# Optimization experiments

Measured on AMD Instinct MI355X. Metric: run time of the kernel, lower is better.

Reference implementation:

```python
import jax, jax.numpy as jnp
import numpy as np

B, N, K, DEG = 128, 4096, 25, 16
BN_EPS = 1e-5


def setup_inputs() -> dict:
    key = jax.random.key(0)
    ks = jax.random.split(key, 16)

    def sp_lap(k, V):
        # fixed-degree random sparse scaled Laplacian (COO); values scaled so the
        # K=25 Chebyshev recursion x2 = 2*L@x1 - x0 stays numerically bounded
        rows = jnp.repeat(jnp.arange(V, dtype=jnp.int32), DEG)
        cols = jax.random.randint(k, (V * DEG,), 0, V, dtype=jnp.int32)
        vals = jax.random.normal(jax.random.fold_in(k, 1), (V * DEG,), jnp.float32) * 0.05
        return rows, cols, vals

    l0_rows, l0_cols, l0_vals = sp_lap(ks[0], N)
    l2_rows, l2_cols, l2_vals = sp_lap(ks[1], N // 4)
    l4_rows, l4_cols, l4_vals = sp_lap(ks[2], N // 16)

    x = jax.random.normal(ks[3], (B, N, 1), jnp.float32)
    w1 = jax.random.normal(ks[4], (1 * K, 32), jnp.float32) * 0.1
    b1 = jnp.zeros((32,), jnp.float32)
    w2 = jax.random.normal(ks[5], (32 * K, 64), jnp.float32) * 0.05
    b2 = jnp.zeros((64,), jnp.float32)
    w3 = jax.random.normal(ks[6], (64 * K, 64), jnp.float32) * 0.05
    b3 = jnp.zeros((64,), jnp.float32)
    fc1_w = jax.random.normal(ks[7], (N // 16 * 64, 512), jnp.float32) * 0.01
    fc1_b = jnp.zeros((512,), jnp.float32)
    bn_gamma = jnp.ones((512,), jnp.float32)
    bn_beta = jnp.zeros((512,), jnp.float32)
    fc2_w = jax.random.normal(ks[8], (512, 10), jnp.float32) * 0.05
    fc2_b = jnp.zeros((10,), jnp.float32)

    return dict(x=x,
                l0_rows=l0_rows, l0_cols=l0_cols, l0_vals=l0_vals,
                l2_rows=l2_rows, l2_cols=l2_cols, l2_vals=l2_vals,
                l4_rows=l4_rows, l4_cols=l4_cols, l4_vals=l4_vals,
                w1=w1, b1=b1, w2=w2, b2=b2, w3=w3, b3=b3,
                fc1_w=fc1_w, fc1_b=fc1_b, bn_gamma=bn_gamma, bn_beta=bn_beta,
                fc2_w=fc2_w, fc2_b=fc2_b)


def spmm(rows, cols, vals, xm, V):
    # sparse (V,V) @ dense (V,M) via gather + segment-sum
    return jax.ops.segment_sum(vals[:, None] * xm[cols], rows, num_segments=V)


def cheb(rows, cols, vals, x, W, b):
    # GCNCheb: Chebyshev polynomial basis T_k(L) x, k=0..K-1, then linear projection
    Bb, V, Fin = x.shape
    Kk = W.shape[0] // Fin
    x0 = jnp.transpose(x, (1, 2, 0)).reshape(V, Fin * Bb)  # (V, Fin*B)
    xs = [x0]
    x1 = spmm(rows, cols, vals, x0, V)
    xs.append(x1)
    for _ in range(2, Kk):
        x2 = 2.0 * spmm(rows, cols, vals, x1, V) - x0
        xs.append(x2)
        x0, x1 = x1, x2
    Xc = jnp.stack(xs, 0).reshape(Kk, V, Fin, Bb)          # (K, V, Fin, B)
    Xc = jnp.transpose(Xc, (3, 1, 2, 0)).reshape(Bb * V, Fin * Kk)
    return (Xc @ W + b).reshape(Bb, V, -1)


def pool4(x):
    # max-pool over consecutive groups of 4 nodes (gcn_pool_4)
    Bb, V, F = x.shape
    return x.reshape(Bb, V // 4, 4, F).max(axis=2)


def reference(x,
              l0_rows, l0_cols, l0_vals,
              l2_rows, l2_cols, l2_vals,
              l4_rows, l4_cols, l4_vals,
              w1, b1, w2, b2, w3, b3,
              fc1_w, fc1_b, bn_gamma, bn_beta, fc2_w, fc2_b):
    h = jax.nn.relu(cheb(l0_rows, l0_cols, l0_vals, x, w1, b1))
    h = pool4(h)                                             # (B, N/4, 32)
    h = jax.nn.relu(cheb(l2_rows, l2_cols, l2_vals, h, w2, b2))
    h = pool4(h)                                             # (B, N/16, 64)
    h = jax.nn.relu(cheb(l4_rows, l4_cols, l4_vals, h, w3, b3))
    h = h.reshape(h.shape[0], -1)                            # (B, N/16 * 64)
    h = h @ fc1_w + fc1_b                                    # (B, 512)
    mean = h.mean(axis=0)
    var = h.var(axis=0)  # biased, matching torch BatchNorm training normalization
    h = (h - mean) / jnp.sqrt(var + BN_EPS) * bn_gamma + bn_beta
    h = jax.nn.relu(h)
    logits = h @ fc2_w + fc2_b                               # (B, 10)
    return jax.nn.log_softmax(logits, axis=1)
```

## Files before the change

kernel.cpp:

```cpp
#include <hip/hip_runtime.h>

#define B_ 128
#define K_ 25
#define DEG_ 16

#define R4(X) X(0) X(1) X(2) X(3)

typedef __attribute__((ext_vector_type(4))) float f32x4;
typedef __attribute__((ext_vector_type(8))) short bf16x8;

__device__ __forceinline__ float4 f4ma(float t, float4 w, float4 a) {
    a.x = fmaf(t, w.x, a.x); a.y = fmaf(t, w.y, a.y);
    a.z = fmaf(t, w.z, a.z); a.w = fmaf(t, w.w, a.w);
    return a;
}
__device__ __forceinline__ float4 f4max(float4 a, float4 b) {
    return make_float4(fmaxf(a.x, b.x), fmaxf(a.y, b.y), fmaxf(a.z, b.z), fmaxf(a.w, b.w));
}
__device__ __forceinline__ unsigned f2bfu(float f) {
    unsigned u = __float_as_uint(f);
    return (u + 0x7FFFu + ((u >> 16) & 1u)) >> 16;
}
__device__ __forceinline__ unsigned packbf(float e, float o) { return f2bfu(e) | (f2bfu(o) << 16); }

__device__ __forceinline__ bf16x8 u2b(uint4 u) {
    union { uint4 u4; bf16x8 b8; } c; c.u4 = u; return c.b8;
}
__device__ __forceinline__ f32x4 mfma_bf(uint4 a, uint4 b, f32x4 c) {
    return __builtin_amdgcn_mfma_f32_16x16x32_bf16(u2b(a), u2b(b), c, 0, 0, 0);
}

__global__ __launch_bounds__(256) void k_transpose_x(const float* __restrict__ x, float* __restrict__ x0) {
    int i = blockIdx.x * 256 + threadIdx.x;
    int v = i >> 7, b = i & 127;
    x0[i] = x[(b << 12) + v];
}

__global__ __launch_bounds__(256) void k_packw(const float* __restrict__ w2, const float* __restrict__ w3,
        unsigned short* __restrict__ wb2, unsigned short* __restrict__ wb3) {
    int i = blockIdx.x * 256 + threadIdx.x;
    if (i < 51200) {
        int k = i >> 11, rem = i & 2047, fo = rem >> 5, fi = rem & 31;
        wb2[i] = (unsigned short)f2bfu(w2[(size_t)(fi * K_ + k) * 64 + fo]);
    }
    if (i < 102400) {
        int k = i >> 12, rem = i & 4095, fo = rem >> 6, fi = rem & 63;
        wb3[i] = (unsigned short)f2bfu(w3[(size_t)(fi * K_ + k) * 64 + fo]);
    }
}

__global__ __launch_bounds__(256) void k_spmm1(const int* __restrict__ cols, const float* __restrict__ vals,
        const float2* __restrict__ cur, const float2* __restrict__ prev,
        float2* __restrict__ next, int two) {
    int t = blockIdx.x * 256 + threadIdx.x;
    int v = __builtin_amdgcn_readfirstlane(t >> 6);
    int lane = threadIdx.x & 63;
    int base = v * DEG_;
    float2 s = make_float2(0.f, 0.f);
#pragma unroll
    for (int d = 0; d < DEG_; ++d) {
        float wv = vals[base + d];
        float2 xx = cur[((size_t)cols[base + d] << 6) + lane];
        s.x = fmaf(wv, xx.x, s.x); s.y = fmaf(wv, xx.y, s.y);
    }
    size_t idx = ((size_t)v << 6) + lane;
    if (two) {
        float2 p = prev[idx];
        s.x = 2.f * s.x - p.x; s.y = 2.f * s.y - p.y;
    }
    next[idx] = s;
}

template<int LOGC4>
__global__ __launch_bounds__(256) void k_spmm4(const int* __restrict__ cols, const float* __restrict__ vals,
                        const float4* __restrict__ cur, const float4* __restrict__ prev,
                        float4* __restrict__ next, unsigned* __restrict__ mir, int two) {
    constexpr int LOGW4 = LOGC4 - 3;
    int xcd = blockIdx.x & 7, q = blockIdx.x >> 3;
    int tid = q * 256 + threadIdx.x;
    int v = __builtin_amdgcn_readfirstlane(tid >> LOGW4);
    int c4 = (xcd << LOGW4) + (tid & ((1 << LOGW4) - 1));
    int base = v * DEG_;
    float4 s = make_float4(0.f, 0.f, 0.f, 0.f);
#pragma unroll
    for (int d = 0; d < DEG_; ++d) {
        float w = vals[base + d];
        float4 xx = cur[((size_t)cols[base + d] << LOGC4) + c4];
        s = f4ma(w, xx, s);
    }
    size_t idx = ((size_t)v << LOGC4) + c4;
    if (two) {
        float4 p = prev[idx];
        s.x = 2.f * s.x - p.x; s.y = 2.f * s.y - p.y;
        s.z = 2.f * s.z - p.z; s.w = 2.f * s.w - p.w;
    }
    next[idx] = s;
    float tx = __shfl_down(s.x, 32), ty = __shfl_down(s.y, 32),
          tz = __shfl_down(s.z, 32), tw = __shfl_down(s.w, 32);
    if ((threadIdx.x & 63) < 32) {
        int c = c4 << 2;
        int fi2 = c >> 8, b0 = c & 127;
        uint4 m = make_uint4(packbf(s.x, tx), packbf(s.y, ty), packbf(s.z, tz), packbf(s.w, tw));
        *(uint4*)(mir + ((size_t)v << (LOGC4 + 1)) + ((size_t)fi2 << 7) + b0) = m;
    }
}

__global__ __launch_bounds__(256) void k_proj1_pool(const float* __restrict__ basis,
        const float* __restrict__ W1, const float* __restrict__ b1, float* __restrict__ pool1,
        unsigned* __restrict__ mir) {
    int half = blockIdx.y;
    int i = blockIdx.x * 256 + threadIdx.x;
    int g = i >> 7, b = i & 127;
    const float* wbase = W1 + half * 16;
#define P1_DM(j) float4 M##j = make_float4(-1e30f, -1e30f, -1e30f, -1e30f);
    R4(P1_DM)
#undef P1_DM
    for (int r = 0; r < 4; ++r) {
        const float* bp = basis + (((size_t)(4 * g + r) << 7) + b);
#define P1_DC(j) float4 C##j = make_float4(0.f, 0.f, 0.f, 0.f);
        R4(P1_DC)
#undef P1_DC
#pragma unroll 5
        for (int k = 0; k < K_; ++k) {
            float tv = bp[(size_t)k * 524288];
            const float4* w = (const float4*)(wbase + k * 32);
#define P1_FM(j) C##j = f4ma(tv, w[j], C##j);
            R4(P1_FM)
#undef P1_FM
        }
#define P1_MX(j) M##j = f4max(M##j, C##j);
        R4(P1_MX)
#undef P1_MX
    }
    float* op = pool1 + ((size_t)g << 12) + ((size_t)half << 11) + b;
    unsigned* mp = mir + ((size_t)g << 11) + ((size_t)half << 10) + b;
    const float* bb = b1 + half * 16;
#define P1_ST(j) { \
    float e0 = fmaxf(M##j.x + bb[4*j+0], 0.f); \
    float o0 = fmaxf(M##j.y + bb[4*j+1], 0.f); \
    float e1 = fmaxf(M##j.z + bb[4*j+2], 0.f); \
    float o1 = fmaxf(M##j.w + bb[4*j+3], 0.f); \
    op[(4*j+0)*128] = e0; op[(4*j+1)*128] = o0; \
    op[(4*j+2)*128] = e1; op[(4*j+3)*128] = o1; \
    mp[(2*j+0)*128] = packbf(e0, o0); \
    mp[(2*j+1)*128] = packbf(e1, o1); }
    R4(P1_ST)
#undef P1_ST
}

__global__ __launch_bounds__(256) void k_proj_l2m(const unsigned* __restrict__ mir, size_t slotH,
        const uint4* __restrict__ wb, float* __restrict__ acc, int k0, int init,
        const float* __restrict__ bias) {
    int wid = blockIdx.x * 4 + (threadIdx.x >> 6);
    int lane = threadIdx.x & 63;
    int lm = lane & 15, lg = lane >> 4;
    int v = wid >> 3, b0 = (wid & 7) << 4;
    float* ap = acc + ((size_t)v << 13) + b0 + (lg << 2);
    f32x4 C0, C1, C2, C3;
    if (init) {
        float q0 = bias[lm], q1 = bias[16 + lm], q2 = bias[32 + lm], q3 = bias[48 + lm];
        C0 = f32x4{q0, q0, q0, q0}; C1 = f32x4{q1, q1, q1, q1};
        C2 = f32x4{q2, q2, q2, q2}; C3 = f32x4{q3, q3, q3, q3};
    } else {
        C0 = *(const f32x4*)(ap + (size_t)lm * 128);
        C1 = *(const f32x4*)(ap + (size_t)(16 + lm) * 128);
        C2 = *(const f32x4*)(ap + (size_t)(32 + lm) * 128);
        C3 = *(const f32x4*)(ap + (size_t)(48 + lm) * 128);
    }
    const unsigned* mp0 = mir + ((size_t)v << 11) + (lg << 9) + b0 + lm;
#pragma unroll
    for (int kk = 0; kk < 5; ++kk) {
        const unsigned* mp = mp0 + (size_t)kk * slotH;
        uint4 a = make_uint4(mp[0], mp[128], mp[256], mp[384]);
        int kb = (k0 + kk) << 6;
        uint4 w0 = wb[(kb + lm) * 4 + lg];
        uint4 w1 = wb[(kb + 16 + lm) * 4 + lg];
        uint4 w2 = wb[(kb + 32 + lm) * 4 + lg];
        uint4 w3 = wb[(kb + 48 + lm) * 4 + lg];
        C0 = mfma_bf(a, w0, C0);
        C1 = mfma_bf(a, w1, C1);
        C2 = mfma_bf(a, w2, C2);
        C3 = mfma_bf(a, w3, C3);
    }
    *(f32x4*)(ap + (size_t)lm * 128) = C0;
    *(f32x4*)(ap + (size_t)(16 + lm) * 128) = C1;
    *(f32x4*)(ap + (size_t)(32 + lm) * 128) = C2;
    *(f32x4*)(ap + (size_t)(48 + lm) * 128) = C3;
}

__global__ __launch_bounds__(256) void k_proj_l3m(const unsigned* __restrict__ mir, size_t slotH,
        const uint4* __restrict__ wb, float* __restrict__ acc, int k0, int init,
        const float* __restrict__ bias, int finalrelu) {
    int wid = blockIdx.x * 4 + (threadIdx.x >> 6);
    int lane = threadIdx.x & 63;
    int lm = lane & 15, lg = lane >> 4;
    int v = wid >> 3, b0 = (wid & 7) << 4;
    float* ap = acc + ((size_t)v << 13) + b0 + (lg << 2);
    f32x4 C0, C1, C2, C3;
    if (init) {
        float q0 = bias[lm], q1 = bias[16 + lm], q2 = bias[32 + lm], q3 = bias[48 + lm];
        C0 = f32x4{q0, q0, q0, q0}; C1 = f32x4{q1, q1, q1, q1};
        C2 = f32x4{q2, q2, q2, q2}; C3 = f32x4{q3, q3, q3, q3};
    } else {
        C0 = *(const f32x4*)(ap + (size_t)lm * 128);
        C1 = *(const f32x4*)(ap + (size_t)(16 + lm) * 128);
        C2 = *(const f32x4*)(ap + (size_t)(32 + lm) * 128);
        C3 = *(const f32x4*)(ap + (size_t)(48 + lm) * 128);
    }
    const unsigned* mp0 = mir + ((size_t)v << 12) + b0 + lm;
#pragma unroll
    for (int kk = 0; kk < 5; ++kk) {
        const unsigned* mp = mp0 + (size_t)kk * slotH;
        int kb = (k0 + kk) << 6;
#pragma unroll
        for (int ks = 0; ks < 2; ++ks) {
            const unsigned* mk = mp + (size_t)((ks << 4) + (lg << 2)) * 128;
            uint4 a = make_uint4(mk[0], mk[128], mk[256], mk[384]);
            int wof = (ks << 2) + lg;
            uint4 w0 = wb[(kb + lm) * 8 + wof];
            uint4 w1 = wb[(kb + 16 + lm) * 8 + wof];
            uint4 w2 = wb[(kb + 32 + lm) * 8 + wof];
            uint4 w3 = wb[(kb + 48 + lm) * 8 + wof];
            C0 = mfma_bf(a, w0, C0);
            C1 = mfma_bf(a, w1, C1);
            C2 = mfma_bf(a, w2, C2);
            C3 = mfma_bf(a, w3, C3);
        }
    }
    if (finalrelu) {
#pragma unroll
        for (int r = 0; r < 4; ++r) {
            C0[r] = fmaxf(C0[r], 0.f); C1[r] = fmaxf(C1[r], 0.f);
            C2[r] = fmaxf(C2[r], 0.f); C3[r] = fmaxf(C3[r], 0.f);
        }
    }
    *(f32x4*)(ap + (size_t)lm * 128) = C0;
    *(f32x4*)(ap + (size_t)(16 + lm) * 128) = C1;
    *(f32x4*)(ap + (size_t)(32 + lm) * 128) = C2;
    *(f32x4*)(ap + (size_t)(48 + lm) * 128) = C3;
}

__global__ __launch_bounds__(256) void k_relu_pool_m(const float* __restrict__ acc,
        float* __restrict__ pool, unsigned* __restrict__ mir) {
    int i = blockIdx.x * 256 + threadIdx.x;
    int g = i >> 12, fi2 = (i >> 7) & 31, b = i & 127;
    const float* ap = acc + (((size_t)g << 2) << 13) + (fi2 << 8) + b;
    float me = 0.f, mo = 0.f;
#pragma unroll
    for (int r = 0; r < 4; ++r) {
        me = fmaxf(me, ap[0]); mo = fmaxf(mo, ap[128]);
        ap += 8192;
    }
    size_t po = ((size_t)g << 13) + (fi2 << 8) + b;
    pool[po] = me; pool[po + 128] = mo;
    mir[i] = packbf(me, mo);
}

__global__ __launch_bounds__(256) void k_fc1_part(const float* __restrict__ t3, const float* __restrict__ w,
                           float* __restrict__ part) {
    int blk = blockIdx.x;
    int bg = blk >> 7;
    int rs = (blk >> 1) & 63;
    int j = ((blk & 1) << 8) + threadIdx.x;
    int b0 = bg << 3;
    float a0=0.f,a1=0.f,a2=0.f,a3=0.f,a4=0.f,a5=0.f,a6=0.f,a7=0.f;
    int r0 = rs << 8;
#pragma unroll 4
    for (int row = r0; row < r0 + 256; ++row) {
        float wv = w[((size_t)row << 9) + j];
        const float4* tp = (const float4*)(t3 + ((size_t)row << 7) + b0);
        float4 t0 = tp[0], t1 = tp[1];
        a0 = fmaf(t0.x, wv, a0);
        a1 = fmaf(t0.y, wv, a1);
        a2 = fmaf(t0.z, wv, a2);
        a3 = fmaf(t0.w, wv, a3);
        a4 = fmaf(t1.x, wv, a4);
        a5 = fmaf(t1.y, wv, a5);
        a6 = fmaf(t1.z, wv, a6);
        a7 = fmaf(t1.w, wv, a7);
    }
    float* pp = part + (((size_t)(rs << 7) + b0) << 9) + j;
    pp[0*512]=a0; pp[1*512]=a1; pp[2*512]=a2; pp[3*512]=a3;
    pp[4*512]=a4; pp[5*512]=a5; pp[6*512]=a6; pp[7*512]=a7;
}

__global__ __launch_bounds__(256) void k_fc1_red(const float* __restrict__ part, const float* __restrict__ bias,
                          float* __restrict__ h) {
    int i = blockIdx.x * 256 + threadIdx.x;
    float a = bias[i & 511];
#pragma unroll 8
    for (int rs = 0; rs < 64; ++rs) a += part[((size_t)rs << 16) + i];
    h[i] = a;
}

__global__ void k_bnstats(const float* __restrict__ h, float* __restrict__ mv) {
    __shared__ float s1[128], s2[128];
    int j = blockIdx.x, t = threadIdx.x;
    float v = h[(size_t)t * 512 + j];
    s1[t] = v; s2[t] = v * v;
    __syncthreads();
    for (int o = 64; o > 0; o >>= 1) {
        if (t < o) { s1[t] += s1[t + o]; s2[t] += s2[t + o]; }
        __syncthreads();
    }
    if (t == 0) {
        float m = s1[0] * (1.f / 128.f);
        float var = s2[0] * (1.f / 128.f) - m * m;
        mv[j] = m;
        mv[512 + j] = rsqrtf(var + 1e-5f);
    }
}

__global__ void k_head(const float* __restrict__ h, const float* __restrict__ mv,
                       const float* __restrict__ gamma, const float* __restrict__ beta,
                       const float* __restrict__ w2, const float* __restrict__ b2,
                       float* __restrict__ out) {
    __shared__ float hr[512];
    __shared__ float lg[16];
    int b = blockIdx.x, t = threadIdx.x;
    for (int j = t; j < 512; j += 64) {
        float x = (h[(size_t)b * 512 + j] - mv[j]) * mv[512 + j] * gamma[j] + beta[j];
        hr[j] = fmaxf(x, 0.f);
    }
    __syncthreads();
    if (t < 10) {
        float a = b2[t];
        for (int j = 0; j < 512; ++j) a += hr[j] * w2[j * 10 + t];
        lg[t] = a;
    }
    __syncthreads();
    if (t == 0) {
        float mx = -1e30f;
        for (int q = 0; q < 10; ++q) mx = fmaxf(mx, lg[q]);
        float sum = 0.f;
        for (int q = 0; q < 10; ++q) sum += expf(lg[q] - mx);
        float ls = logf(sum) + mx;
        for (int q = 0; q < 10; ++q) out[b * 10 + q] = lg[q] - ls;
    }
}

extern "C" void kernel_launch(void* const* d_in, const int* in_sizes, int n_in,
                              void* d_out, int out_size, void* d_ws, size_t ws_size,
                              hipStream_t stream) {
    (void)in_sizes; (void)n_in; (void)out_size; (void)ws_size;
    const float* x      = (const float*)d_in[0];
    const int*   l0cols = (const int*)d_in[2];
    const float* l0vals = (const float*)d_in[3];
    const int*   l2cols = (const int*)d_in[5];
    const float* l2vals = (const float*)d_in[6];
    const int*   l4cols = (const int*)d_in[8];
    const float* l4vals = (const float*)d_in[9];
    const float* w1   = (const float*)d_in[10];
    const float* b1   = (const float*)d_in[11];
    const float* w2   = (const float*)d_in[12];
    const float* b2   = (const float*)d_in[13];
    const float* w3   = (const float*)d_in[14];
    const float* b3   = (const float*)d_in[15];
    const float* fc1w = (const float*)d_in[16];
    const float* fc1b = (const float*)d_in[17];
    const float* gam  = (const float*)d_in[18];
    const float* bet  = (const float*)d_in[19];
    const float* fc2w = (const float*)d_in[20];
    const float* fc2b = (const float*)d_in[21];
    float* out = (float*)d_out;

    const size_t S1 = 4096 * 128;
    const size_t S2 = 1024 * 4096;
    const size_t S3 = 256 * 8192;
    const int CKP = 5;

    float* ws = (float*)d_ws;
    float* basis1 = ws;
    float* ring2f = ws + 25 * S1;
    unsigned* mir2 = (unsigned*)(ring2f + 3 * S2);
    float* tailp  = (float*)(mir2 + (size_t)CKP * (S2 / 2));
    float* h      = tailp;
    float* mv     = h + 65536;
    unsigned short* wb2 = (unsigned short*)(mv + 1024);
    unsigned short* wb3 = wb2 + 51200;
    float* acc2   = basis1;
    float* ring3f = ring2f;
    float* acc3   = ring2f + 3 * S3;
    unsigned* mir3 = mir2;
    float* part   = basis1;

    k_packw<<<400, 256, 0, stream>>>(w2, w3, wb2, wb3);

    k_transpose_x<<<2048, 256, 0, stream>>>(x, basis1);
    for (int k = 1; k < 25; ++k) {
        const float* cur  = basis1 + (size_t)(k - 1) * S1;
        const float* prev = (k >= 2) ? basis1 + (size_t)(k - 2) * S1 : cur;
        float* next = basis1 + (size_t)k * S1;
        k_spmm1<<<1024, 256, 0, stream>>>(l0cols, l0vals, (const float2*)cur,
                                          (const float2*)prev, (float2*)next, k >= 2 ? 1 : 0);
    }
    k_proj1_pool<<<dim3(512, 2), 256, 0, stream>>>(basis1, w1, b1, ring2f, mir2);

    {
        int cs = 0;
        for (int k = 0; k < 25; ++k) {
            if (k >= 1) {
                const float* cur  = ring2f + (size_t)((k - 1) % 3) * S2;
                const float* prev = ring2f + (size_t)((k >= 2 ? k - 2 : 0) % 3) * S2;
                float* next = ring2f + (size_t)(k % 3) * S2;
                unsigned* mirp = mir2 + (size_t)(k % CKP) * (S2 / 2);
                k_spmm4<10><<<4096, 256, 0, stream>>>(l2cols, l2vals, (const float4*)cur,
                                                      (const float4*)prev, (float4*)next,
                                                      mirp, k >= 2 ? 1 : 0);
            }
            if (k - cs + 1 == CKP) {
                k_proj_l2m<<<2048, 256, 0, stream>>>(mir2, S2 / 2, (const uint4*)wb2, acc2, cs,
                                                     cs == 0 ? 1 : 0, b2);
                cs = k + 1;
            }
        }
    }
    k_relu_pool_m<<<4096, 256, 0, stream>>>(acc2, ring3f , mir3 );

    {
        int cs = 0;
        for (int k = 0; k < 25; ++k) {
            if (k >= 1) {
                const float* cur  = ring3f + (size_t)((k - 1) % 3) * S3;
                const float* prev = ring3f + (size_t)((k >= 2 ? k - 2 : 0) % 3) * S3;
                float* next = ring3f + (size_t)(k % 3) * S3;
                unsigned* mirp = mir3 + (size_t)(k % CKP) * (S3 / 2);
                k_spmm4<11><<<2048, 256, 0, stream>>>(l4cols, l4vals, (const float4*)cur,
                                                      (const float4*)prev, (float4*)next,
                                                      mirp, k >= 2 ? 1 : 0);
            }
            if (k - cs + 1 == CKP) {
                k_proj_l3m<<<512, 256, 0, stream>>>(mir3, S3 / 2, (const uint4*)wb3, acc3, cs,
                                                    cs == 0 ? 1 : 0, b3, cs == 20 ? 1 : 0);
                cs = k + 1;
            }
        }
    }

    k_fc1_part<<<2048, 256, 0, stream>>>(acc3, fc1w, part);
    k_fc1_red<<<256, 256, 0, stream>>>(part, fc1b, h);
    k_bnstats<<<512, 128, 0, stream>>>(h, mv);
    k_head<<<128, 64, 0, stream>>>(h, mv, gam, bet, fc2w, fc2b, out);
}
```

Baseline: 919.0 us.

## Run Chebyshev recursion for layers 2-3 in LDS-resident column slices across steps

Replaces the per-step global-memory SpMM launches for the layer 2 and layer 3 Chebyshev recursions with chain kernels. Each block keeps a column slice of the current and previous basis in shared memory and advances several recursion steps before writing the state back. Data layouts of the pooled activations and the bf16 mirror buffers are reorganised into per-slice blocks, and the projection kernels are re-indexed to match. This cuts repeated global reads and writes of the full basis plus launch count, at the cost of 64KB LDS per block, lower occupancy and fewer blocks (512/256).

```diff
diff --git a/kernel.cpp b/kernel.cpp
--- a/kernel.cpp
+++ b/kernel.cpp
@@ -17,6 +17,9 @@
 __device__ __forceinline__ float4 f4max(float4 a, float4 b) {
     return make_float4(fmaxf(a.x, b.x), fmaxf(a.y, b.y), fmaxf(a.z, b.z), fmaxf(a.w, b.w));
 }
+__device__ __forceinline__ float4 f4sub2(float4 s, float4 p) {
+    return make_float4(2.f * s.x - p.x, 2.f * s.y - p.y, 2.f * s.z - p.z, 2.f * s.w - p.w);
+}
 __device__ __forceinline__ unsigned f2bfu(float f) {
     unsigned u = __float_as_uint(f);
     return (u + 0x7FFFu + ((u >> 16) & 1u)) >> 16;
@@ -29,6 +32,7 @@
 __device__ __forceinline__ f32x4 mfma_bf(uint4 a, uint4 b, f32x4 c) {
     return __builtin_amdgcn_mfma_f32_16x16x32_bf16(u2b(a), u2b(b), c, 0, 0, 0);
 }
+
 
 __global__ __launch_bounds__(256) void k_transpose_x(const float* __restrict__ x, float* __restrict__ x0) {
     int i = blockIdx.x * 256 + threadIdx.x;
@@ -71,42 +75,143 @@
     next[idx] = s;
 }
 
-template<int LOGC4>
-__global__ __launch_bounds__(256) void k_spmm4(const int* __restrict__ cols, const float* __restrict__ vals,
-                        const float4* __restrict__ cur, const float4* __restrict__ prev,
-                        float4* __restrict__ next, unsigned* __restrict__ mir, int two) {
-    constexpr int LOGW4 = LOGC4 - 3;
-    int xcd = blockIdx.x & 7, q = blockIdx.x >> 3;
-    int tid = q * 256 + threadIdx.x;
-    int v = __builtin_amdgcn_readfirstlane(tid >> LOGW4);
-    int c4 = (xcd << LOGW4) + (tid & ((1 << LOGW4) - 1));
-    int base = v * DEG_;
-    float4 s = make_float4(0.f, 0.f, 0.f, 0.f);
-#pragma unroll
-    for (int d = 0; d < DEG_; ++d) {
-        float w = vals[base + d];
-        float4 xx = cur[((size_t)cols[base + d] << LOGC4) + c4];
-        s = f4ma(w, xx, s);
-    }
-    size_t idx = ((size_t)v << LOGC4) + c4;
-    if (two) {
-        float4 p = prev[idx];
-        s.x = 2.f * s.x - p.x; s.y = 2.f * s.y - p.y;
-        s.z = 2.f * s.z - p.z; s.w = 2.f * s.w - p.w;
-    }
-    next[idx] = s;
-    float tx = __shfl_down(s.x, 32), ty = __shfl_down(s.y, 32),
-          tz = __shfl_down(s.z, 32), tw = __shfl_down(s.w, 32);
-    if ((threadIdx.x & 63) < 32) {
-        int c = c4 << 2;
-        int fi2 = c >> 8, b0 = c & 127;
-        uint4 m = make_uint4(packbf(s.x, tx), packbf(s.y, ty), packbf(s.z, tz), packbf(s.w, tw));
-        *(uint4*)(mir + ((size_t)v << (LOGC4 + 1)) + ((size_t)fi2 << 7) + b0) = m;
-    }
+__global__ __launch_bounds__(256) void k_chain2(const int* __restrict__ cols, const float* __restrict__ vals,
+        float* __restrict__ stA, float* __restrict__ stB, unsigned* __restrict__ mir,
+        int k0, int nsteps) {
+    __shared__ float st[2][8192];
+    int s = blockIdx.x, t = threadIdx.x;
+    size_t sb = (size_t)s * 8192;
+#pragma unroll
+    for (int r = 0; r < 4; ++r) {
+        int v = t + (r << 8);
+        *(float4*)&st[0][v*8]     = *(const float4*)(stA + sb + v*8);
+        *(float4*)&st[0][v*8 + 4] = *(const float4*)(stA + sb + v*8 + 4);
+        *(float4*)&st[1][v*8]     = *(const float4*)(stB + sb + v*8);
+        *(float4*)&st[1][v*8 + 4] = *(const float4*)(stB + sb + v*8 + 4);
+    }
+    __syncthreads();
+    int pc = 0, pb = 1;
+    for (int step = 0; step < nsteps; ++step) {
+        int k = k0 + step;
+        float4 n0_0, n1_0, n0_1, n1_1, n0_2, n1_2, n0_3, n1_3;
+#define C2_CMP(r, N0, N1) { \
+        int v = t + (r << 8); \
+        const int4* cp = (const int4*)(cols + v * 16); \
+        const float4* vp = (const float4*)(vals + v * 16); \
+        float4 a0 = make_float4(0.f,0.f,0.f,0.f), a1 = a0; \
+        for (int dd = 0; dd < 4; ++dd) { \
+            int4 cc = cp[dd]; float4 ww = vp[dd]; \
+            const float* p; \
+            p = &st[pc][cc.x * 8]; a0 = f4ma(ww.x, *(const float4*)p, a0); a1 = f4ma(ww.x, *(const float4*)(p+4), a1); \
+            p = &st[pc][cc.y * 8]; a0 = f4ma(ww.y, *(const float4*)p, a0); a1 = f4ma(ww.y, *(const float4*)(p+4), a1); \
+            p = &st[pc][cc.z * 8]; a0 = f4ma(ww.z, *(const float4*)p, a0); a1 = f4ma(ww.z, *(const float4*)(p+4), a1); \
+            p = &st[pc][cc.w * 8]; a0 = f4ma(ww.w, *(const float4*)p, a0); a1 = f4ma(ww.w, *(const float4*)(p+4), a1); \
+        } \
+        if (k >= 2) { \
+            float4 p0 = *(const float4*)&st[pb][v*8], p1 = *(const float4*)&st[pb][v*8+4]; \
+            a0 = f4sub2(a0, p0); a1 = f4sub2(a1, p1); \
+        } \
+        N0 = a0; N1 = a1; }
+        C2_CMP(0, n0_0, n1_0)
+        C2_CMP(1, n0_1, n1_1)
+        C2_CMP(2, n0_2, n1_2)
+        C2_CMP(3, n0_3, n1_3)
+#undef C2_CMP
+        __syncthreads();
+        unsigned* ms = mir + (size_t)(k % 5) * 2097152 + (size_t)s * 4096;
+#define C2_ST(r, N0, N1) { \
+        int v = t + (r << 8); \
+        *(float4*)&st[pb][v*8] = N0; *(float4*)&st[pb][v*8+4] = N1; \
+        uint4 mw = make_uint4(packbf(N0.x, N1.x), packbf(N0.y, N1.y), packbf(N0.z, N1.z), packbf(N0.w, N1.w)); \
+        *(uint4*)(ms + v * 4) = mw; }
+        C2_ST(0, n0_0, n1_0)
+        C2_ST(1, n0_1, n1_1)
+        C2_ST(2, n0_2, n1_2)
+        C2_ST(3, n0_3, n1_3)
+#undef C2_ST
+        __syncthreads();
+        int tmp = pc; pc = pb; pb = tmp;
+    }
+#pragma unroll
+    for (int r = 0; r < 4; ++r) {
+        int v = t + (r << 8);
+        *(float4*)(stA + sb + v*8)     = *(const float4*)&st[pc][v*8];
+        *(float4*)(stA + sb + v*8 + 4) = *(const float4*)&st[pc][v*8+4];
+        *(float4*)(stB + sb + v*8)     = *(const float4*)&st[pb][v*8];
+        *(float4*)(stB + sb + v*8 + 4) = *(const float4*)&st[pb][v*8+4];
+    }
+}
+
+__global__ __launch_bounds__(512) void k_chain3(const int* __restrict__ cols, const float* __restrict__ vals,
+        float* __restrict__ stA, float* __restrict__ stB, unsigned* __restrict__ mir,
+        int k0, int nsteps) {
+    __shared__ float st[2][8192];
+    int s = blockIdx.x, t = threadIdx.x;
+    int v = t >> 1, h = t & 1;
+    int o0 = v * 32 + h * 8;
+    size_t sb = (size_t)s * 8192;
+    *(float4*)&st[0][o0]      = *(const float4*)(stA + sb + o0);
+    *(float4*)&st[0][o0 + 4]  = *(const float4*)(stA + sb + o0 + 4);
+    *(float4*)&st[0][o0 + 16] = *(const float4*)(stA + sb + o0 + 16);
+    *(float4*)&st[0][o0 + 20] = *(const float4*)(stA + sb + o0 + 20);
+    *(float4*)&st[1][o0]      = *(const float4*)(stB + sb + o0);
+    *(float4*)&st[1][o0 + 4]  = *(const float4*)(stB + sb + o0 + 4);
+    *(float4*)&st[1][o0 + 16] = *(const float4*)(stB + sb + o0 + 16);
+    *(float4*)&st[1][o0 + 20] = *(const float4*)(stB + sb + o0 + 20);
+    __syncthreads();
+    int pc = 0, pb = 1;
+    const int4* cp = (const int4*)(cols + v * 16);
+    const float4* vp = (const float4*)(vals + v * 16);
+    for (int step = 0; step < nsteps; ++step) {
+        int k = k0 + step;
+        float4 ae0 = make_float4(0.f,0.f,0.f,0.f), ae1 = ae0, ao0 = ae0, ao1 = ae0;
+        for (int dd = 0; dd < 4; ++dd) {
+            int4 cc = cp[dd]; float4 ww = vp[dd];
+            const float* p;
+            p = &st[pc][cc.x * 32 + h * 8];
+            ae0 = f4ma(ww.x, *(const float4*)p, ae0);       ae1 = f4ma(ww.x, *(const float4*)(p+4), ae1);
+            ao0 = f4ma(ww.x, *(const float4*)(p+16), ao0);  ao1 = f4ma(ww.x, *(const float4*)(p+20), ao1);
+            p = &st[pc][cc.y * 32 + h * 8];
+            ae0 = f4ma(ww.y, *(const float4*)p, ae0);       ae1 = f4ma(ww.y, *(const float4*)(p+4), ae1);
+            ao0 = f4ma(ww.y, *(const float4*)(p+16), ao0);  ao1 = f4ma(ww.y, *(const float4*)(p+20), ao1);
+            p = &st[pc][cc.z * 32 + h * 8];
+            ae0 = f4ma(ww.z, *(const float4*)p, ae0);       ae1 = f4ma(ww.z, *(const float4*)(p+4), ae1);
+            ao0 = f4ma(ww.z, *(const float4*)(p+16), ao0);  ao1 = f4ma(ww.z, *(const float4*)(p+20), ao1);
+            p = &st[pc][cc.w * 32 + h * 8];
+            ae0 = f4ma(ww.w, *(const float4*)p, ae0);       ae1 = f4ma(ww.w, *(const float4*)(p+4), ae1);
+            ao0 = f4ma(ww.w, *(const float4*)(p+16), ao0);  ao1 = f4ma(ww.w, *(const float4*)(p+20), ao1);
+        }
+        if (k >= 2) {
+            ae0 = f4sub2(ae0, *(const float4*)&st[pb][o0]);
+            ae1 = f4sub2(ae1, *(const float4*)&st[pb][o0 + 4]);
+            ao0 = f4sub2(ao0, *(const float4*)&st[pb][o0 + 16]);
+            ao1 = f4sub2(ao1, *(const float4*)&st[pb][o0 + 20]);
+        }
+        __syncthreads();
+        *(float4*)&st[pb][o0]      = ae0;
+        *(float4*)&st[pb][o0 + 4]  = ae1;
+        *(float4*)&st[pb][o0 + 16] = ao0;
+        *(float4*)&st[pb][o0 + 20] = ao1;
+        unsigned* ms = mir + (size_t)(k % 5) * 1048576 + (size_t)s * 4096 + v * 16 + h * 8;
+        uint4 w0 = make_uint4(packbf(ae0.x, ao0.x), packbf(ae0.y, ao0.y), packbf(ae0.z, ao0.z), packbf(ae0.w, ao0.w));
+        uint4 w1 = make_uint4(packbf(ae1.x, ao1.x), packbf(ae1.y, ao1.y), packbf(ae1.z, ao1.z), packbf(ae1.w, ao1.w));
+        *(uint4*)(ms) = w0;
+        *(uint4*)(ms + 4) = w1;
+        __syncthreads();
+        int tmp = pc; pc = pb; pb = tmp;
+    }
+    *(float4*)(stA + sb + o0)      = *(const float4*)&st[pc][o0];
+    *(float4*)(stA + sb + o0 + 4)  = *(const float4*)&st[pc][o0 + 4];
+    *(float4*)(stA + sb + o0 + 16) = *(const float4*)&st[pc][o0 + 16];
+    *(float4*)(stA + sb + o0 + 20) = *(const float4*)&st[pc][o0 + 20];
+    *(float4*)(stB + sb + o0)      = *(const float4*)&st[pb][o0];
+    *(float4*)(stB + sb + o0 + 4)  = *(const float4*)&st[pb][o0 + 4];
+    *(float4*)(stB + sb + o0 + 16) = *(const float4*)&st[pb][o0 + 16];
+    *(float4*)(stB + sb + o0 + 20) = *(const float4*)&st[pb][o0 + 20];
 }
 
 __global__ __launch_bounds__(256) void k_proj1_pool(const float* __restrict__ basis,
-        const float* __restrict__ W1, const float* __restrict__ b1, float* __restrict__ pool1,
+        const float* __restrict__ W1, const float* __restrict__ b1, float* __restrict__ st2,
         unsigned* __restrict__ mir) {
     int half = blockIdx.y;
     int i = blockIdx.x * 256 + threadIdx.x;
@@ -132,18 +237,19 @@
         R4(P1_MX)
 #undef P1_MX
     }
-    float* op = pool1 + ((size_t)g << 12) + ((size_t)half << 11) + b;
-    unsigned* mp = mir + ((size_t)g << 11) + ((size_t)half << 10) + b;
     const float* bb = b1 + half * 16;
+    int bq = b >> 2, bo = b & 3;
 #define P1_ST(j) { \
     float e0 = fmaxf(M##j.x + bb[4*j+0], 0.f); \
     float o0 = fmaxf(M##j.y + bb[4*j+1], 0.f); \
     float e1 = fmaxf(M##j.z + bb[4*j+2], 0.f); \
     float o1 = fmaxf(M##j.w + bb[4*j+3], 0.f); \
-    op[(4*j+0)*128] = e0; op[(4*j+1)*128] = o0; \
-    op[(4*j+2)*128] = e1; op[(4*j+3)*128] = o1; \
-    mp[(2*j+0)*128] = packbf(e0, o0); \
-    mp[(2*j+1)*128] = packbf(e1, o1); }
+    int f2a = half * 8 + 2 * j; \
+    float* sa = st2 + ((size_t)(f2a * 32 + bq)) * 8192 + g * 8 + bo; \
+    float* sbp = st2 + ((size_t)((f2a + 1) * 32 + bq)) * 8192 + g * 8 + bo; \
+    sa[0] = e0; sa[4] = o0; sbp[0] = e1; sbp[4] = o1; \
+    mir[((size_t)(f2a * 32 + bq)) * 4096 + g * 4 + bo] = packbf(e0, o0); \
+    mir[((size_t)((f2a + 1) * 32 + bq)) * 4096 + g * 4 + bo] = packbf(e1, o1); }
     R4(P1_ST)
 #undef P1_ST
 }
@@ -167,11 +273,12 @@
         C2 = *(const f32x4*)(ap + (size_t)(32 + lm) * 128);
         C3 = *(const f32x4*)(ap + (size_t)(48 + lm) * 128);
     }
-    const unsigned* mp0 = mir + ((size_t)v << 11) + (lg << 9) + b0 + lm;
+    int b = b0 + lm;
+    const unsigned* mp0 = mir + ((size_t)((lg << 2) * 32 + (b >> 2))) * 4096 + (size_t)v * 4 + (b & 3);
 #pragma unroll
     for (int kk = 0; kk < 5; ++kk) {
         const unsigned* mp = mp0 + (size_t)kk * slotH;
-        uint4 a = make_uint4(mp[0], mp[128], mp[256], mp[384]);
+        uint4 a = make_uint4(mp[0], mp[131072], mp[262144], mp[393216]);
         int kb = (k0 + kk) << 6;
         uint4 w0 = wb[(kb + lm) * 4 + lg];
         uint4 w1 = wb[(kb + 16 + lm) * 4 + lg];
@@ -207,15 +314,16 @@
         C2 = *(const f32x4*)(ap + (size_t)(32 + lm) * 128);
         C3 = *(const f32x4*)(ap + (size_t)(48 + lm) * 128);
     }
-    const unsigned* mp0 = mir + ((size_t)v << 12) + b0 + lm;
+    int bq4 = wid & 7;
+    const unsigned* mp0 = mir + (size_t)v * 16 + lm;
 #pragma unroll
     for (int kk = 0; kk < 5; ++kk) {
-        const unsigned* mp = mp0 + (size_t)kk * slotH;
+        const unsigned* mpk = mp0 + (size_t)kk * slotH;
         int kb = (k0 + kk) << 6;
 #pragma unroll
         for (int ks = 0; ks < 2; ++ks) {
-            const unsigned* mk = mp + (size_t)((ks << 4) + (lg << 2)) * 128;
-            uint4 a = make_uint4(mk[0], mk[128], mk[256], mk[384]);
+            const unsigned* mk = mpk + ((size_t)(((ks << 4) + (lg << 2)) * 8 + bq4)) * 4096;
+            uint4 a = make_uint4(mk[0], mk[32768], mk[65536], mk[98304]);
             int wof = (ks << 2) + lg;
             uint4 w0 = wb[(kb + lm) * 8 + wof];
             uint4 w1 = wb[(kb + 16 + lm) * 8 + wof];
@@ -241,7 +349,7 @@
 }
 
 __global__ __launch_bounds__(256) void k_relu_pool_m(const float* __restrict__ acc,
-        float* __restrict__ pool, unsigned* __restrict__ mir) {
+        float* __restrict__ st3, unsigned* __restrict__ mir) {
     int i = blockIdx.x * 256 + threadIdx.x;
     int g = i >> 12, fi2 = (i >> 7) & 31, b = i & 127;
     const float* ap = acc + (((size_t)g << 2) << 13) + (fi2 << 8) + b;
@@ -251,9 +359,10 @@
         me = fmaxf(me, ap[0]); mo = fmaxf(mo, ap[128]);
         ap += 8192;
     }
-    size_t po = ((size_t)g << 13) + (fi2 << 8) + b;
-    pool[po] = me; pool[po + 128] = mo;
-    mir[i] = packbf(me, mo);
+    int s = fi2 * 8 + (b >> 4), bo = b & 15;
+    st3[(size_t)s * 8192 + g * 32 + bo] = me;
+    st3[(size_t)s * 8192 + g * 32 + 16 + bo] = mo;
+    mir[(size_t)s * 4096 + g * 16 + bo] = packbf(me, mo);
 }
 
 __global__ __launch_bounds__(256) void k_fc1_part(const float* __restrict__ t3, const float* __restrict__ w,
@@ -367,20 +476,20 @@
     const size_t S1 = 4096 * 128;
     const size_t S2 = 1024 * 4096;
     const size_t S3 = 256 * 8192;
-    const int CKP = 5;
 
     float* ws = (float*)d_ws;
     float* basis1 = ws;
-    float* ring2f = ws + 25 * S1;
-    unsigned* mir2 = (unsigned*)(ring2f + 3 * S2);
-    float* tailp  = (float*)(mir2 + (size_t)CKP * (S2 / 2));
-    float* h      = tailp;
+    float* st2A   = ws + 25 * S1;
+    float* st2B   = st2A + S2;
+    unsigned* mir2 = (unsigned*)(st2B + S2);
+    float* acc3   = (float*)(mir2 + 5 * (S2 / 2));
+    float* h      = acc3 + S3;
     float* mv     = h + 65536;
     unsigned short* wb2 = (unsigned short*)(mv + 1024);
     unsigned short* wb3 = wb2 + 51200;
     float* acc2   = basis1;
-    float* ring3f = ring2f;
-    float* acc3   = ring2f + 3 * S3;
+    float* st3A   = st2A;
+    float* st3B   = st2B;
     unsigned* mir3 = mir2;
     float* part   = basis1;
 
@@ -394,47 +503,23 @@
         k_spmm1<<<1024, 256, 0, stream>>>(l0cols, l0vals, (const float2*)cur,
                                           (const float2*)prev, (float2*)next, k >= 2 ? 1 : 0);
     }
-    k_proj1_pool<<<dim3(512, 2), 256, 0, stream>>>(basis1, w1, b1, ring2f, mir2);
-
-    {
-        int cs = 0;
-        for (int k = 0; k < 25; ++k) {
-            if (k >= 1) {
-                const float* cur  = ring2f + (size_t)((k - 1) % 3) * S2;
-                const float* prev = ring2f + (size_t)((k >= 2 ? k - 2 : 0) % 3) * S2;
-                float* next = ring2f + (size_t)(k % 3) * S2;
-                unsigned* mirp = mir2 + (size_t)(k % CKP) * (S2 / 2);
-                k_spmm4<10><<<4096, 256, 0, stream>>>(l2cols, l2vals, (const float4*)cur,
-                                                      (const float4*)prev, (float4*)next,
-                                                      mirp, k >= 2 ? 1 : 0);
-            }
-            if (k - cs + 1 == CKP) {
-                k_proj_l2m<<<2048, 256, 0, stream>>>(mir2, S2 / 2, (const uint4*)wb2, acc2, cs,
-                                                     cs == 0 ? 1 : 0, b2);
-                cs = k + 1;
-            }
-        }
-    }
-    k_relu_pool_m<<<4096, 256, 0, stream>>>(acc2, ring3f , mir3 );
-
-    {
-        int cs = 0;
-        for (int k = 0; k < 25; ++k) {
-            if (k >= 1) {
-                const float* cur  = ring3f + (size_t)((k - 1) % 3) * S3;
-                const float* prev = ring3f + (size_t)((k >= 2 ? k - 2 : 0) % 3) * S3;
-                float* next = ring3f + (size_t)(k % 3) * S3;
-                unsigned* mirp = mir3 + (size_t)(k % CKP) * (S3 / 2);
-                k_spmm4<11><<<2048, 256, 0, stream>>>(l4cols, l4vals, (const float4*)cur,
-                                                      (const float4*)prev, (float4*)next,
-                                                      mirp, k >= 2 ? 1 : 0);
-            }
-            if (k - cs + 1 == CKP) {
-                k_proj_l3m<<<512, 256, 0, stream>>>(mir3, S3 / 2, (const uint4*)wb3, acc3, cs,
-                                                    cs == 0 ? 1 : 0, b3, cs == 20 ? 1 : 0);
-                cs = k + 1;
-            }
-        }
+    k_proj1_pool<<<dim3(512, 2), 256, 0, stream>>>(basis1, w1, b1, st2A, mir2);
+
+    for (int c = 0; c < 5; ++c) {
+        int kk0 = (c == 0) ? 1 : 5 * c;
+        int ns  = (c == 0) ? 4 : 5;
+        k_chain2<<<512, 256, 0, stream>>>(l2cols, l2vals, st2A, st2B, mir2, kk0, ns);
+        k_proj_l2m<<<2048, 256, 0, stream>>>(mir2, S2 / 2, (const uint4*)wb2, acc2, 5 * c,
+                                             c == 0 ? 1 : 0, b2);
+    }
+    k_relu_pool_m<<<4096, 256, 0, stream>>>(acc2, st3A, mir3);
+
+    for (int c = 0; c < 5; ++c) {
+        int kk0 = (c == 0) ? 1 : 5 * c;
+        int ns  = (c == 0) ? 4 : 5;
+        k_chain3<<<256, 512, 0, stream>>>(l4cols, l4vals, st3A, st3B, mir3, kk0, ns);
+        k_proj_l3m<<<512, 256, 0, stream>>>(mir3, S3 / 2, (const uint4*)wb3, acc3, 5 * c,
+                                            c == 0 ? 1 : 0, b3, c == 4 ? 1 : 0);
     }
 
     k_fc1_part<<<2048, 256, 0, stream>>>(acc3, fc1w, part);
```

Measured after the change: 959.1 us. +4.4%, slower.
